# Performance work log

Hardware: AMD Instinct MI355X
Metric: run time of the kernel (lower is better)

Reference implementation:

```python
import jax, jax.numpy as jnp
import numpy as np

GROUPS = 32
EPS = 1e-6

def groupnorm(x, gamma, beta):
    b, c, h, w = x.shape
    xg = x.reshape(b, GROUPS, c // GROUPS, h, w)
    mu = xg.mean(axis=(2, 3, 4), keepdims=True)
    var = xg.var(axis=(2, 3, 4), keepdims=True)
    xn = ((xg - mu) / jnp.sqrt(var + EPS)).reshape(b, c, h, w)
    return xn * gamma[None, :, None, None] + beta[None, :, None, None]

def conv1x1(x, w, b):
    return jnp.einsum('oc,bchw->bohw', w, x) + b[None, :, None, None]

def attn_branch(xn, wq, bq, wk, bk, v_flat, scale):
    q = conv1x1(xn, wq, bq)
    k = conv1x1(xn, wk, bk)
    b_, c, h, w = q.shape
    qf = q.reshape(b_, c, h * w)   # b c n
    kf = k.reshape(b_, c, h * w)   # b c n
    scores = jnp.einsum('bci,bcj->bij', qf, kf) * scale  # b n n
    attn = jax.nn.softmax(scores, axis=2)
    out = jnp.einsum('bcj,bij->bci', v_flat, attn)       # b c n
    return out.reshape(b_, c, h, w)

def setup_inputs() -> dict:
    key = jax.random.key(0)
    ks = jax.random.split(key, 14)
    B, C, H, W = 4, 64, 64, 64
    R = C // 16  # SE reduction
    s = 0.05
    return {
        'x1': jax.random.normal(ks[0], (B, C, H, W), jnp.float32),
        'x2': jax.random.normal(ks[1], (B, C, H, W), jnp.float32),
        'se_w1': jax.random.normal(ks[2], (R, C), jnp.float32) * s,
        'se_w2': jax.random.normal(ks[3], (C, R), jnp.float32) * s,
        'gn_gamma': jnp.ones((C,), jnp.float32),
        'gn_beta': jnp.zeros((C,), jnp.float32),
        'wq': jax.random.normal(ks[4], (C, C), jnp.float32) * s,
        'bq': jnp.zeros((C,), jnp.float32),
        'wk': jax.random.normal(ks[5], (C, C), jnp.float32) * s,
        'bk': jnp.zeros((C,), jnp.float32),
        'wv': jax.random.normal(ks[6], (C, C), jnp.float32) * s,
        'bv': jnp.zeros((C,), jnp.float32),
    }

def reference(x1, x2, se_w1, se_w2, gn_gamma, gn_beta, wq, bq, wk, bk, wv, bv):
    x = x1 + x2
    # SE channel attention (ends in sigmoid), then an EXTRA sigmoid as in source
    y = x.mean(axis=(2, 3))                         # b c
    y = jax.nn.relu(y @ se_w1.T)                    # b r
    y = jax.nn.sigmoid(y @ se_w2.T)                 # b c
    se = x * y[:, :, None, None]
    ch_w = jax.nn.sigmoid(se)
    xn = groupnorm(x, gn_gamma, gn_beta)
    v = conv1x1(xn, wv, bv)
    b_, c, h, w = v.shape
    v_flat = v.reshape(b_, c, h * w)
    scale = 1.0 / jnp.sqrt(jnp.float32(c))
    # source reuses q1/k1 convs for BOTH branches
    h1 = attn_branch(groupnorm(x1, gn_gamma, gn_beta), wq, bq, wk, bk, v_flat, scale)
    h2 = attn_branch(groupnorm(x2, gn_gamma, gn_beta), wq, bq, wk, bk, v_flat, scale)
    return 2.0 * h1 * ch_w + 2.0 * h2 * (1.0 - ch_w)
```

## Files before the change

kernel.cpp:

```cpp
#include <hip/hip_runtime.h>

#define STATS_OFF 0
#define AD_OFF    20480
#define SEY_OFF   26624
#define BIAS_OFF  27648
#define WQB_OFF   32768
#define WKB_OFF   40960
#define WVB_OFF   49152
#define Q_OFF     57344
#define K_OFF     (Q_OFF + 4194304)
#define V_OFF     (K_OFF + 4194304)
#define PO_OFF    (V_OFF + 2097152)

#define QSCALE 0.18033688f

typedef __attribute__((ext_vector_type(8))) short  short8;
typedef __attribute__((ext_vector_type(4))) short  s16x4;
typedef __attribute__((ext_vector_type(2))) unsigned int u32x2;
typedef __attribute__((ext_vector_type(4))) float  f32x4;

#if __has_builtin(__builtin_amdgcn_mfma_f32_16x16x16bf16_1k)
#define HAS_1K 1
#else
#define HAS_1K 0
#endif

#if __has_builtin(__builtin_amdgcn_exp2f)
__device__ inline float fexp2(float x) { return __builtin_amdgcn_exp2f(x); }
#else
__device__ inline float fexp2(float x) { return exp2f(x); }
#endif

__device__ inline ushort f2b(float f) {
  return (ushort)((__float_as_uint(f) + 0x8000u) >> 16);
}
__device__ inline unsigned pack2(float x, float y) {
  unsigned ux = __float_as_uint(x) + 0x8000u;
  unsigned uy = __float_as_uint(y) + 0x8000u;
  return __builtin_amdgcn_perm(uy, ux, 0x07060302);
}
__device__ inline float b2f(ushort u) { return __uint_as_float(((unsigned)u) << 16); }

__device__ inline f32x4 mfma16(short8 a, short8 b, f32x4 c) {
  return __builtin_amdgcn_mfma_f32_16x16x32_bf16(a, b, c, 0, 0, 0);
}

__device__ inline float wsum64(float v) {
  #pragma unroll
  for (int o = 32; o > 0; o >>= 1) v += __shfl_down(v, o, 64);
  return v;
}

__global__ __launch_bounds__(256) void sc_stats(const float* __restrict__ x1,
                                                const float* __restrict__ x2,
                                                float* __restrict__ stats) {
  int blk = blockIdx.x;
  int bc = blk >> 2, chunk = blk & 3;
  const float4* p1 = (const float4*)(x1 + (size_t)bc * 4096 + chunk * 1024);
  const float4* p2 = (const float4*)(x2 + (size_t)bc * 4096 + chunk * 1024);
  float4 a = p1[threadIdx.x], b = p2[threadIdx.x];
  float s1 = a.x + a.y + a.z + a.w;
  float q1 = a.x*a.x + a.y*a.y + a.z*a.z + a.w*a.w;
  float s2 = b.x + b.y + b.z + b.w;
  float q2 = b.x*b.x + b.y*b.y + b.z*b.z + b.w*b.w;
  float p12 = a.x*b.x + a.y*b.y + a.z*b.z + a.w*b.w;
  s1 = wsum64(s1); q1 = wsum64(q1); s2 = wsum64(s2); q2 = wsum64(q2); p12 = wsum64(p12);
  __shared__ float red[4][5];
  int w = threadIdx.x >> 6, ln = threadIdx.x & 63;
  if (ln == 0) { red[w][0] = s1; red[w][1] = q1; red[w][2] = s2; red[w][3] = q2; red[w][4] = p12; }
  __syncthreads();
  if (threadIdx.x < 5) {
    float acc = 0;
    #pragma unroll
    for (int ww = 0; ww < 4; ww++) acc += red[ww][threadIdx.x];
    stats[(size_t)blk * 5 + threadIdx.x] = acc;
  }
}

__global__ __launch_bounds__(256) void sc_prep(const float* __restrict__ stats,
                                               const float* __restrict__ w1,
                                               const float* __restrict__ w2,
                                               const float* __restrict__ gamma,
                                               const float* __restrict__ beta,
                                               const float* __restrict__ wq, const float* __restrict__ bq,
                                               const float* __restrict__ wk, const float* __restrict__ bk,
                                               const float* __restrict__ wv, const float* __restrict__ bv,
                                               float* __restrict__ ad, float* __restrict__ sey,
                                               float* __restrict__ biasbuf,
                                               ushort* __restrict__ wqb, ushort* __restrict__ wkb,
                                               ushort* __restrict__ wvb) {
  int t = threadIdx.x; int b = t >> 6, c = t & 63;
  float s1 = 0, q1 = 0, s2 = 0, q2 = 0, p12 = 0;
  #pragma unroll
  for (int ch = 0; ch < 4; ch++) {
    const float* sp = stats + (size_t)(t * 4 + ch) * 5;
    s1 += sp[0]; q1 += sp[1]; s2 += sp[2]; q2 += sp[3]; p12 += sp[4];
  }
  float sx = s1 + s2, qx = q1 + q2 + 2.f * p12;
  __shared__ float smu[256], sS[3][256], sQ[3][256], sy[16], sdd[3][256];
  smu[t] = sx * (1.f / 4096.f);
  sS[0][t] = sx; sQ[0][t] = qx; sS[1][t] = s1; sQ[1][t] = q1; sS[2][t] = s2; sQ[2][t] = q2;
  __syncthreads();
  if (t < 16) {
    int bb = t >> 2, r = t & 3; float acc = 0.f;
    for (int cc = 0; cc < 64; cc++) acc += w1[r*64+cc] * smu[bb*64+cc];
    sy[t] = fmaxf(acc, 0.f);
  }
  __syncthreads();
  float acc = 0.f;
  #pragma unroll
  for (int r = 0; r < 4; r++) acc += w2[c*4+r] * sy[b*4+r];
  sey[t] = 1.f / (1.f + fexp2(-acc * 1.44269504f));
  int prt = t ^ 1;
  float g = gamma[c], bt = beta[c];
  #pragma unroll
  for (int s = 0; s < 3; s++) {
    float S = sS[s][t] + sS[s][prt], Q = sQ[s][t] + sQ[s][prt];
    float mean = S * (1.f / 8192.f);
    float var  = Q * (1.f / 8192.f) - mean * mean;
    float rstd = rsqrtf(var + 1e-6f);
    float a = g * rstd;
    float d = bt - mean * a;
    ad[((s*256) + t)*2 + 0] = a;
    ad[((s*256) + t)*2 + 1] = d;
    sdd[s][t] = d;
  }
  __syncthreads();
  #pragma unroll
  for (int k = 0; k < 5; k++) {
    int idx = k * 256 + t;
    const float* W; const float* bs; const float* dd; int o; float scale = 1.f;
    if (idx < 256)      { int bb = idx >> 6; o = idx & 63; W = wv; bs = bv; dd = &sdd[0][bb*64]; }
    else if (idx < 768) { int r = idx - 256; int bh = r >> 6; o = r & 63; W = wq; bs = bq;
                          dd = &sdd[1 + (bh & 1)][(bh >> 1)*64]; scale = QSCALE; }
    else                { int r = idx - 768; int bh = r >> 6; o = r & 63; W = wk; bs = bk;
                          dd = &sdd[1 + (bh & 1)][(bh >> 1)*64]; }
    float a2 = bs[o];
    for (int cc = 0; cc < 64; cc++) a2 += W[o*64+cc] * dd[cc];
    biasbuf[idx] = a2 * scale;
  }
  for (int i = t; i < 4096; i += 256) {
    wqb[i] = f2b(wq[i] * QSCALE);
    wkb[i] = f2b(wk[i]);
    wvb[i] = f2b(wv[i]);
  }
}

__global__ __launch_bounds__(256) void sc_proj(const float* __restrict__ x1, const float* __restrict__ x2,
    const float* __restrict__ ad, const float* __restrict__ biasbuf,
    const ushort* __restrict__ wqb, const ushort* __restrict__ wkb, const ushort* __restrict__ wvb,
    ushort* __restrict__ qout, ushort* __restrict__ kout, ushort* __restrict__ vout) {
  int pt = blockIdx.x, src = blockIdx.y, b = blockIdx.z, t = threadIdx.x;
  __shared__ ushort xlds[64 * 66];
  __shared__ ushort olds[64 * 66];
  __shared__ float sbias[2][64];
  if (t < 128) {
    int proj = t >> 6, o = t & 63;
    float bb;
    if (src == 0) bb = (proj == 0) ? biasbuf[b*64 + o] : 0.f;
    else          bb = biasbuf[256 + (proj ? 512 : 0) + (b*2 + src - 1)*64 + o];
    sbias[proj][o] = bb;
  }
  {
    int c = t >> 2, pq = (t & 3) * 16;
    const float* px1 = x1 + ((size_t)(b*64 + c))*4096 + pt*64 + pq;
    const float* px2 = x2 + ((size_t)(b*64 + c))*4096 + pt*64 + pq;
    float av = ad[((src*256) + b*64 + c)*2 + 0];
    #pragma unroll
    for (int k4 = 0; k4 < 4; k4++) {
      float4 v1 = *(const float4*)(px1 + 4*k4);
      float xv[4];
      if (src == 1) { xv[0]=v1.x; xv[1]=v1.y; xv[2]=v1.z; xv[3]=v1.w; }
      else {
        float4 v2 = *(const float4*)(px2 + 4*k4);
        if (src == 2) { xv[0]=v2.x; xv[1]=v2.y; xv[2]=v2.z; xv[3]=v2.w; }
        else { xv[0]=v1.x+v2.x; xv[1]=v1.y+v2.y; xv[2]=v1.z+v2.z; xv[3]=v1.w+v2.w; }
      }
      #pragma unroll
      for (int k = 0; k < 4; k++)
        xlds[(pq + 4*k4 + k)*66 + c] = f2b(av * xv[k]);
    }
  }
  __syncthreads();
  int wave = t >> 6, lane = t & 63, quad = lane >> 4, l15 = lane & 15;
  int orow = t >> 2, ocol = (t & 3) * 16;
  if (src == 0) {
    const ushort* ap = wvb + (wave*16 + l15)*64 + quad*8;
    short8 a0 = *(const short8*)ap;
    short8 a1 = *(const short8*)(ap + 32);
    f32x4 cinit;
    #pragma unroll
    for (int r = 0; r < 4; r++) cinit[r] = sbias[0][wave*16 + quad*4 + r];
    #pragma unroll
    for (int s = 0; s < 4; s++) {
      const ushort* bp = xlds + (s*16 + l15)*66 + quad*8;
      short8 b0 = *(const short8*)bp;
      short8 b1 = *(const short8*)(bp + 32);
      f32x4 acc = mfma16(a0, b0, cinit);
      acc = mfma16(a1, b1, acc);
      #pragma unroll
      for (int r = 0; r < 4; r++)
        olds[(wave*16 + quad*4 + r)*66 + s*16 + l15] = f2b(acc[r]);
    }
    __syncthreads();
    uint4 w0 = *(const uint4*)&olds[orow*66 + ocol];
    uint4 w1 = *(const uint4*)&olds[orow*66 + ocol + 8];
    ushort* dst = vout + ((size_t)(b*64 + orow))*4096 + pt*64 + ocol;
    *(uint4*)dst = w0; *(uint4*)(dst + 8) = w1;
  } else {
    int bh = b*2 + (src - 1);
    const ushort* ap = xlds + (wave*16 + l15)*66 + quad*8;
    short8 a0 = *(const short8*)ap;
    short8 a1 = *(const short8*)(ap + 32);
    #pragma unroll
    for (int proj = 0; proj < 2; proj++) {
      const ushort* Wb = proj == 0 ? wqb : wkb;
      ushort* dst = proj == 0 ? qout : kout;
      #pragma unroll
      for (int s = 0; s < 4; s++) {
        const ushort* bp = Wb + (s*16 + l15)*64 + quad*8;
        short8 b0 = *(const short8*)bp;
        short8 b1 = *(const short8*)(bp + 32);
        float bb = sbias[proj][s*16 + l15];
        f32x4 acc = {bb, bb, bb, bb};
        acc = mfma16(a0, b0, acc);
        acc = mfma16(a1, b1, acc);
        #pragma unroll
        for (int r = 0; r < 4; r++)
          olds[(wave*16 + quad*4 + r)*66 + s*16 + l15] = f2b(acc[r]);
      }
      __syncthreads();
      uint4 w0 = *(const uint4*)&olds[orow*66 + ocol];
      uint4 w1 = *(const uint4*)&olds[orow*66 + ocol + 8];
      ushort* dp = dst + ((size_t)bh*4096 + pt*64 + orow)*64 + ocol;
      *(uint4*)dp = w0; *(uint4*)(dp + 8) = w1;
      if (proj == 0) __syncthreads();
    }
  }
}

__global__ __launch_bounds__(256, 4) void sc_flash(const ushort* __restrict__ qg,
                                                   const ushort* __restrict__ kg,
                                                   const ushort* __restrict__ vg,
                                                   ushort* __restrict__ po,
                                                   float* __restrict__ pl,
                                                   int jsbits) {
  int blk = blockIdx.x;
  int bh = blk & 7, rest = blk >> 3;
  int njs = 1 << jsbits, njt = 64 >> jsbits;
  int js = rest & (njs - 1), itile = rest >> jsbits;
  int jbase = js * (njt << 6);
  int b = bh >> 1;
  int t = threadIdx.x, wave = t >> 6, lane = t & 63, quad = lane >> 4, l15 = lane & 15;
  int i0 = itile * 128 + wave * 32;

  __shared__ ushort Klds[64 * 72];
  __shared__ ushort Vlds[64 * 72];
#if !HAS_1K
  __shared__ ushort Plds[4][32 * 72];
#endif

  const ushort* qbase = qg + ((size_t)bh * 4096 + i0 + l15) * 64 + quad * 8;
  short8 Qb[2][2];
  Qb[0][0] = *(const short8*)qbase;
  Qb[0][1] = *(const short8*)(qbase + 32);
  Qb[1][0] = *(const short8*)(qbase + 16 * 64);
  Qb[1][1] = *(const short8*)(qbase + 16 * 64 + 32);

  f32x4 O[2][4]; const f32x4 zero4 = {0.f, 0.f, 0.f, 0.f};
  #pragma unroll
  for (int ib = 0; ib < 2; ib++)
    #pragma unroll
    for (int cb = 0; cb < 4; cb++) O[ib][cb] = zero4;
  float lsum[2] = {0.f, 0.f};

  int sr = t >> 2, sc = (t & 3) * 16;
  const ushort* ksrc = kg + ((size_t)bh * 4096 + jbase + sr) * 64 + sc;
  const ushort* vsrc = vg + ((size_t)(b * 64 + sr)) * 4096 + jbase + sc;
  ushort* kdst = Klds + sr * 72 + sc;
  ushort* vdst = Vlds + sr * 72 + sc;

  uint4 kr0 = *(const uint4*)ksrc, kr1 = *(const uint4*)(ksrc + 8);
  uint4 vr0 = *(const uint4*)vsrc, vr1 = *(const uint4*)(vsrc + 8);
  ksrc += 4096; vsrc += 64;

  #pragma unroll 1
  for (int jt = 0; jt < njt; jt++) {
    __syncthreads();
    *(uint4*)kdst = kr0; *(uint4*)(kdst + 8) = kr1;
    *(uint4*)vdst = vr0; *(uint4*)(vdst + 8) = vr1;
    __syncthreads();
    if (jt + 1 < njt) {
      kr0 = *(const uint4*)ksrc; kr1 = *(const uint4*)(ksrc + 8);
      vr0 = *(const uint4*)vsrc; vr1 = *(const uint4*)(vsrc + 8);
      ksrc += 4096; vsrc += 64;
    }

    f32x4 S[2][4];
    #pragma unroll
    for (int s = 0; s < 4; s++) {
      const ushort* kp = Klds + (s * 16 + l15) * 72 + quad * 8;
      short8 ka0 = *(const short8*)kp;
      short8 ka1 = *(const short8*)(kp + 32);
      #pragma unroll
      for (int ib = 0; ib < 2; ib++) {
        f32x4 acc = mfma16(ka0, Qb[ib][0], zero4);
        S[ib][s] = mfma16(ka1, Qb[ib][1], acc);
      }
    }

#if HAS_1K
    s16x4 Pb[2][4];
#endif
    #pragma unroll
    for (int ib = 0; ib < 2; ib++) {
      #pragma unroll
      for (int s = 0; s < 4; s++) {
        float p0 = fexp2(S[ib][s][0]);
        float p1 = fexp2(S[ib][s][1]);
        float p2 = fexp2(S[ib][s][2]);
        float p3 = fexp2(S[ib][s][3]);
        lsum[ib] += (p0 + p1) + (p2 + p3);
#if HAS_1K
        u32x2 wpk = {pack2(p0, p1), pack2(p2, p3)};
        Pb[ib][s] = __builtin_bit_cast(s16x4, wpk);
#else
        ushort* pw = &Plds[wave][(ib * 16 + l15) * 72 + s * 16 + quad * 4];
        pw[0] = f2b(p0); pw[1] = f2b(p1); pw[2] = f2b(p2); pw[3] = f2b(p3);
#endif
      }
    }

#if HAS_1K
    #pragma unroll
    for (int s = 0; s < 4; s++) {
      #pragma unroll
      for (int cb = 0; cb < 4; cb++) {
        s16x4 vb = *(const s16x4*)(Vlds + (cb * 16 + l15) * 72 + s * 16 + quad * 4);
        O[0][cb] = __builtin_amdgcn_mfma_f32_16x16x16bf16_1k(Pb[0][s], vb, O[0][cb], 0, 0, 0);
        O[1][cb] = __builtin_amdgcn_mfma_f32_16x16x16bf16_1k(Pb[1][s], vb, O[1][cb], 0, 0, 0);
      }
    }
#else
    __threadfence_block();
    #pragma unroll
    for (int ib = 0; ib < 2; ib++) {
      short8 pa0 = *(const short8*)&Plds[wave][(ib * 16 + l15) * 72 + quad * 8];
      short8 pa1 = *(const short8*)&Plds[wave][(ib * 16 + l15) * 72 + quad * 8 + 32];
      #pragma unroll
      for (int cb = 0; cb < 4; cb++) {
        const ushort* vbp = Vlds + (cb * 16 + l15) * 72 + quad * 8;
        short8 v0 = *(const short8*)vbp;
        short8 v1 = *(const short8*)(vbp + 32);
        O[ib][cb] = mfma16(pa0, v0, O[ib][cb]);
        O[ib][cb] = mfma16(pa1, v1, O[ib][cb]);
      }
    }
#endif
  }

  size_t slice = (size_t)(bh * njs + js) * 4096;
  #pragma unroll
  for (int ib = 0; ib < 2; ib++) {
    float lv = lsum[ib];
    lv += __shfl_xor(lv, 16, 64);
    lv += __shfl_xor(lv, 32, 64);
    if (quad == 0) pl[slice + i0 + ib * 16 + l15] = lv;
    #pragma unroll
    for (int cb = 0; cb < 4; cb++)
      #pragma unroll
      for (int r = 0; r < 4; r++)
        po[(slice + i0 + ib * 16 + quad * 4 + r) * 64 + cb * 16 + l15] = f2b(O[ib][cb][r]);
  }
}

__global__ __launch_bounds__(256) void sc_combine(const float* __restrict__ x1, const float* __restrict__ x2,
                                                  const ushort* __restrict__ po, const float* __restrict__ pl,
                                                  const float* __restrict__ sey,
                                                  float* __restrict__ out, int jsbits) {
  int njs = 1 << jsbits;
  int itile = blockIdx.x, b = blockIdx.y, ch = blockIdx.z, t = threadIdx.x;
  __shared__ float hl[2][32 * 65];
  #pragma unroll
  for (int head = 0; head < 2; head++) {
    int bh = b * 2 + head;
    int i = t >> 2, c8 = (t & 3) * 8;
    float sum[8];
    #pragma unroll
    for (int k = 0; k < 8; k++) sum[k] = 0.f;
    float lacc = 0.f;
    for (int js = 0; js < njs; js++) {
      size_t base = ((size_t)(bh * njs + js)) * 4096;
      uint4 u = *(const uint4*)(po + base * 64 + (size_t)(itile * 64 + i) * 64 + ch * 32 + c8);
      const ushort* us = (const ushort*)&u;
      #pragma unroll
      for (int k = 0; k < 8; k++) sum[k] += b2f(us[k]);
      lacc += pl[base + itile * 64 + i];
    }
    float inv = 1.f / lacc;
    #pragma unroll
    for (int k = 0; k < 8; k++) hl[head][(c8 + k) * 65 + i] = sum[k] * inv;
  }
  __syncthreads();
  #pragma unroll
  for (int it = 0; it < 8; it++) {
    int idx = it * 256 + t;
    int cl = idx >> 6, p = idx & 63;
    int c = ch * 32 + cl;
    size_t gi = ((size_t)(b * 64 + c)) * 4096 + itile * 64 + p;
    float xv = x1[gi] + x2[gi];
    float sig = 1.f / (1.f + fexp2(-xv * sey[b * 64 + c] * 1.44269504f));
    float h1 = hl[0][cl * 65 + p], h2 = hl[1][cl * 65 + p];
    out[gi] = 2.f * (h1 * sig + h2 * (1.f - sig));
  }
}

extern "C" void kernel_launch(void* const* d_in, const int* in_sizes, int n_in,
                              void* d_out, int out_size, void* d_ws, size_t ws_size,
                              hipStream_t stream) {
  (void)in_sizes; (void)n_in; (void)out_size;
  const float* x1    = (const float*)d_in[0];
  const float* x2    = (const float*)d_in[1];
  const float* se_w1 = (const float*)d_in[2];
  const float* se_w2 = (const float*)d_in[3];
  const float* gamma = (const float*)d_in[4];
  const float* beta  = (const float*)d_in[5];
  const float* wq    = (const float*)d_in[6];
  const float* bq    = (const float*)d_in[7];
  const float* wk    = (const float*)d_in[8];
  const float* bk    = (const float*)d_in[9];
  const float* wv    = (const float*)d_in[10];
  const float* bv    = (const float*)d_in[11];
  float* out = (float*)d_out;
  char* ws = (char*)d_ws;
  float*  stats = (float*)(ws + STATS_OFF);
  float*  ad    = (float*)(ws + AD_OFF);
  float*  sey   = (float*)(ws + SEY_OFF);
  float*  biasb = (float*)(ws + BIAS_OFF);
  ushort* wqb   = (ushort*)(ws + WQB_OFF);
  ushort* wkb   = (ushort*)(ws + WKB_OFF);
  ushort* wvb   = (ushort*)(ws + WVB_OFF);
  ushort* qb    = (ushort*)(ws + Q_OFF);
  ushort* kb    = (ushort*)(ws + K_OFF);
  ushort* vb    = (ushort*)(ws + V_OFF);

  int jsbits = 1;
  for (int jb = 3; jb >= 2; jb--) {
    size_t need = (size_t)PO_OFF + ((size_t)8 * 4096 * 64 * 2 + (size_t)8 * 4096 * 4) * (1u << jb);
    if (ws_size >= need) { jsbits = jb; break; }
  }
  int njs = 1 << jsbits;
  ushort* pob = (ushort*)(ws + PO_OFF);
  float*  plb = (float*)(ws + PO_OFF + (size_t)8 * njs * 4096 * 64 * 2);

  sc_stats  <<<1024, 256, 0, stream>>>(x1, x2, stats);
  sc_prep   <<<1, 256, 0, stream>>>(stats, se_w1, se_w2, gamma, beta,
                                    wq, bq, wk, bk, wv, bv,
                                    ad, sey, biasb, wqb, wkb, wvb);
  sc_proj   <<<dim3(64, 3, 4), 256, 0, stream>>>(x1, x2, ad, biasb,
                                                 wqb, wkb, wvb, qb, kb, vb);
  sc_flash  <<<8 * 32 * njs, 256, 0, stream>>>(qb, kb, vb, pob, plb, jsbits);
  sc_combine<<<dim3(64, 4, 2), 256, 0, stream>>>(x1, x2, pob, plb, sey, out, jsbits);
}
```

Baseline: 178.8 us.

## Enlarge flash query tile, swizzle LDS, and redistribute weight prep across kernels

```diff
diff --git a/kernel.cpp b/kernel.cpp
--- a/kernel.cpp
+++ b/kernel.cpp
@@ -3,7 +3,6 @@
 #define STATS_OFF 0
 #define AD_OFF    20480
 #define SEY_OFF   26624
-#define BIAS_OFF  27648
 #define WQB_OFF   32768
 #define WKB_OFF   40960
 #define WVB_OFF   49152
@@ -13,17 +12,12 @@
 #define PO_OFF    (V_OFF + 2097152)
 
 #define QSCALE 0.18033688f
+#define SWZ(r) ((((r) & 7) << 3) ^ (((r) & 8) << 1))
 
 typedef __attribute__((ext_vector_type(8))) short  short8;
 typedef __attribute__((ext_vector_type(4))) short  s16x4;
 typedef __attribute__((ext_vector_type(2))) unsigned int u32x2;
 typedef __attribute__((ext_vector_type(4))) float  f32x4;
-
-#if __has_builtin(__builtin_amdgcn_mfma_f32_16x16x16bf16_1k)
-#define HAS_1K 1
-#else
-#define HAS_1K 0
-#endif
 
 #if __has_builtin(__builtin_amdgcn_exp2f)
 __device__ inline float fexp2(float x) { return __builtin_amdgcn_exp2f(x); }
@@ -53,7 +47,13 @@
 
 __global__ __launch_bounds__(256) void sc_stats(const float* __restrict__ x1,
                                                 const float* __restrict__ x2,
-                                                float* __restrict__ stats) {
+                                                float* __restrict__ stats,
+                                                const float* __restrict__ wq,
+                                                const float* __restrict__ wk,
+                                                const float* __restrict__ wv,
+                                                ushort* __restrict__ wqb,
+                                                ushort* __restrict__ wkb,
+                                                ushort* __restrict__ wvb) {
   int blk = blockIdx.x;
   int bc = blk >> 2, chunk = blk & 3;
   const float4* p1 = (const float4*)(x1 + (size_t)bc * 4096 + chunk * 1024);
@@ -75,6 +75,13 @@
     for (int ww = 0; ww < 4; ww++) acc += red[ww][threadIdx.x];
     stats[(size_t)blk * 5 + threadIdx.x] = acc;
   }
+  if (blk >= 976) {
+    int idx = (blk - 976) * 256 + threadIdx.x;
+    int arr = idx >> 12, e = idx & 4095;
+    if (arr == 0)      wqb[e] = f2b(wq[e] * QSCALE);
+    else if (arr == 1) wkb[e] = f2b(wk[e]);
+    else               wvb[e] = f2b(wv[e]);
+  }
 }
 
 __global__ __launch_bounds__(256) void sc_prep(const float* __restrict__ stats,
@@ -82,13 +89,7 @@
                                                const float* __restrict__ w2,
                                                const float* __restrict__ gamma,
                                                const float* __restrict__ beta,
-                                               const float* __restrict__ wq, const float* __restrict__ bq,
-                                               const float* __restrict__ wk, const float* __restrict__ bk,
-                                               const float* __restrict__ wv, const float* __restrict__ bv,
-                                               float* __restrict__ ad, float* __restrict__ sey,
-                                               float* __restrict__ biasbuf,
-                                               ushort* __restrict__ wqb, ushort* __restrict__ wkb,
-                                               ushort* __restrict__ wvb) {
+                                               float* __restrict__ ad, float* __restrict__ sey) {
   int t = threadIdx.x; int b = t >> 6, c = t & 63;
   float s1 = 0, q1 = 0, s2 = 0, q2 = 0, p12 = 0;
   #pragma unroll
@@ -97,7 +98,7 @@
     s1 += sp[0]; q1 += sp[1]; s2 += sp[2]; q2 += sp[3]; p12 += sp[4];
   }
   float sx = s1 + s2, qx = q1 + q2 + 2.f * p12;
-  __shared__ float smu[256], sS[3][256], sQ[3][256], sy[16], sdd[3][256];
+  __shared__ float smu[256], sS[3][256], sQ[3][256], sy[16];
   smu[t] = sx * (1.f / 4096.f);
   sS[0][t] = sx; sQ[0][t] = qx; sS[1][t] = s1; sQ[1][t] = q1; sS[2][t] = s2; sQ[2][t] = q2;
   __syncthreads();
@@ -120,47 +121,24 @@
     float var  = Q * (1.f / 8192.f) - mean * mean;
     float rstd = rsqrtf(var + 1e-6f);
     float a = g * rstd;
-    float d = bt - mean * a;
     ad[((s*256) + t)*2 + 0] = a;
-    ad[((s*256) + t)*2 + 1] = d;
-    sdd[s][t] = d;
-  }
-  __syncthreads();
-  #pragma unroll
-  for (int k = 0; k < 5; k++) {
-    int idx = k * 256 + t;
-    const float* W; const float* bs; const float* dd; int o; float scale = 1.f;
-    if (idx < 256)      { int bb = idx >> 6; o = idx & 63; W = wv; bs = bv; dd = &sdd[0][bb*64]; }
-    else if (idx < 768) { int r = idx - 256; int bh = r >> 6; o = r & 63; W = wq; bs = bq;
-                          dd = &sdd[1 + (bh & 1)][(bh >> 1)*64]; scale = QSCALE; }
-    else                { int r = idx - 768; int bh = r >> 6; o = r & 63; W = wk; bs = bk;
-                          dd = &sdd[1 + (bh & 1)][(bh >> 1)*64]; }
-    float a2 = bs[o];
-    for (int cc = 0; cc < 64; cc++) a2 += W[o*64+cc] * dd[cc];
-    biasbuf[idx] = a2 * scale;
-  }
-  for (int i = t; i < 4096; i += 256) {
-    wqb[i] = f2b(wq[i] * QSCALE);
-    wkb[i] = f2b(wk[i]);
-    wvb[i] = f2b(wv[i]);
+    ad[((s*256) + t)*2 + 1] = bt - mean * a;
   }
 }
 
 __global__ __launch_bounds__(256) void sc_proj(const float* __restrict__ x1, const float* __restrict__ x2,
-    const float* __restrict__ ad, const float* __restrict__ biasbuf,
+    const float* __restrict__ ad,
+    const float* __restrict__ wq, const float* __restrict__ bq,
+    const float* __restrict__ wk, const float* __restrict__ bk,
+    const float* __restrict__ wv, const float* __restrict__ bv,
     const ushort* __restrict__ wqb, const ushort* __restrict__ wkb, const ushort* __restrict__ wvb,
     ushort* __restrict__ qout, ushort* __restrict__ kout, ushort* __restrict__ vout) {
   int pt = blockIdx.x, src = blockIdx.y, b = blockIdx.z, t = threadIdx.x;
   __shared__ ushort xlds[64 * 66];
   __shared__ ushort olds[64 * 66];
-  __shared__ float sbias[2][64];
-  if (t < 128) {
-    int proj = t >> 6, o = t & 63;
-    float bb;
-    if (src == 0) bb = (proj == 0) ? biasbuf[b*64 + o] : 0.f;
-    else          bb = biasbuf[256 + (proj ? 512 : 0) + (b*2 + src - 1)*64 + o];
-    sbias[proj][o] = bb;
-  }
+  __shared__ float sd[64], sbias[2][64];
+  if (t < 64) sd[t] = ad[((src*256) + b*64 + t)*2 + 1];
+  __syncthreads();
   {
     int c = t >> 2, pq = (t & 3) * 16;
     const float* px1 = x1 + ((size_t)(b*64 + c))*4096 + pt*64 + pq;
@@ -180,6 +158,16 @@
       for (int k = 0; k < 4; k++)
         xlds[(pq + 4*k4 + k)*66 + c] = f2b(av * xv[k]);
     }
+  }
+  int nbias = (src == 0) ? 64 : 128;
+  if (t < nbias) {
+    int proj = t >> 6, o = t & 63;
+    const float* W  = (src == 0) ? wv : (proj == 0 ? wq : wk);
+    const float* bs = (src == 0) ? bv : (proj == 0 ? bq : bk);
+    float acc = bs[o];
+    for (int cc = 0; cc < 64; cc++) acc += W[o*64+cc] * sd[cc];
+    if (src != 0 && proj == 0) acc *= QSCALE;
+    sbias[proj][o] = acc;
   }
   __syncthreads();
   int wave = t >> 6, lane = t & 63, quad = lane >> 4, l15 = lane & 15;
@@ -239,7 +227,7 @@
   }
 }
 
-__global__ __launch_bounds__(256, 4) void sc_flash(const ushort* __restrict__ qg,
+__global__ __launch_bounds__(256, 2) void sc_flash(const ushort* __restrict__ qg,
                                                    const ushort* __restrict__ kg,
                                                    const ushort* __restrict__ vg,
                                                    ushort* __restrict__ po,
@@ -252,33 +240,35 @@
   int jbase = js * (njt << 6);
   int b = bh >> 1;
   int t = threadIdx.x, wave = t >> 6, lane = t & 63, quad = lane >> 4, l15 = lane & 15;
-  int i0 = itile * 128 + wave * 32;
-
-  __shared__ ushort Klds[64 * 72];
-  __shared__ ushort Vlds[64 * 72];
-#if !HAS_1K
-  __shared__ ushort Plds[4][32 * 72];
-#endif
-
-  const ushort* qbase = qg + ((size_t)bh * 4096 + i0 + l15) * 64 + quad * 8;
-  short8 Qb[2][2];
-  Qb[0][0] = *(const short8*)qbase;
-  Qb[0][1] = *(const short8*)(qbase + 32);
-  Qb[1][0] = *(const short8*)(qbase + 16 * 64);
-  Qb[1][1] = *(const short8*)(qbase + 16 * 64 + 32);
-
-  f32x4 O[2][4]; const f32x4 zero4 = {0.f, 0.f, 0.f, 0.f};
-  #pragma unroll
-  for (int ib = 0; ib < 2; ib++)
+  int i0 = itile * 256 + wave * 64;
+
+  __shared__ ushort Klds[64 * 64];
+  __shared__ ushort Vlds[64 * 64];
+
+  short8 Qb[4][2];
+  #pragma unroll
+  for (int ib = 0; ib < 4; ib++) {
+    const ushort* qp = qg + ((size_t)bh * 4096 + i0 + ib * 16 + l15) * 64 + quad * 8;
+    Qb[ib][0] = *(const short8*)qp;
+    Qb[ib][1] = *(const short8*)(qp + 32);
+  }
+
+  f32x4 O[4][4]; const f32x4 zero4 = {0.f, 0.f, 0.f, 0.f};
+  #pragma unroll
+  for (int ib = 0; ib < 4; ib++)
     #pragma unroll
     for (int cb = 0; cb < 4; cb++) O[ib][cb] = zero4;
-  float lsum[2] = {0.f, 0.f};
+  float lsum[4] = {0.f, 0.f, 0.f, 0.f};
 
   int sr = t >> 2, sc = (t & 3) * 16;
+  int swzs = SWZ(sr);
+  int swzl = SWZ(l15);
   const ushort* ksrc = kg + ((size_t)bh * 4096 + jbase + sr) * 64 + sc;
   const ushort* vsrc = vg + ((size_t)(b * 64 + sr)) * 4096 + jbase + sc;
-  ushort* kdst = Klds + sr * 72 + sc;
-  ushort* vdst = Vlds + sr * 72 + sc;
+  ushort* kd0 = Klds + sr * 64 + (sc ^ swzs);
+  ushort* kd1 = Klds + sr * 64 + ((sc + 8) ^ swzs);
+  ushort* vd0 = Vlds + sr * 64 + (sc ^ swzs);
+  ushort* vd1 = Vlds + sr * 64 + ((sc + 8) ^ swzs);
 
   uint4 kr0 = *(const uint4*)ksrc, kr1 = *(const uint4*)(ksrc + 8);
   uint4 vr0 = *(const uint4*)vsrc, vr1 = *(const uint4*)(vsrc + 8);
@@ -287,8 +277,8 @@
   #pragma unroll 1
   for (int jt = 0; jt < njt; jt++) {
     __syncthreads();
-    *(uint4*)kdst = kr0; *(uint4*)(kdst + 8) = kr1;
-    *(uint4*)vdst = vr0; *(uint4*)(vdst + 8) = vr1;
+    *(uint4*)kd0 = kr0; *(uint4*)kd1 = kr1;
+    *(uint4*)vd0 = vr0; *(uint4*)vd1 = vr1;
     __syncthreads();
     if (jt + 1 < njt) {
       kr0 = *(const uint4*)ksrc; kr1 = *(const uint4*)(ksrc + 8);
@@ -296,72 +286,40 @@
       ksrc += 4096; vsrc += 64;
     }
 
-    f32x4 S[2][4];
     #pragma unroll
     for (int s = 0; s < 4; s++) {
-      const ushort* kp = Klds + (s * 16 + l15) * 72 + quad * 8;
-      short8 ka0 = *(const short8*)kp;
-      short8 ka1 = *(const short8*)(kp + 32);
-      #pragma unroll
-      for (int ib = 0; ib < 2; ib++) {
+      int rowK = (s * 16 + l15) * 64;
+      short8 ka0 = *(const short8*)&Klds[rowK + ((quad * 8) ^ swzl)];
+      short8 ka1 = *(const short8*)&Klds[rowK + ((quad * 8 + 32) ^ swzl)];
+      f32x4 S[4];
+      #pragma unroll
+      for (int ib = 0; ib < 4; ib++) {
         f32x4 acc = mfma16(ka0, Qb[ib][0], zero4);
-        S[ib][s] = mfma16(ka1, Qb[ib][1], acc);
+        S[ib] = mfma16(ka1, Qb[ib][1], acc);
       }
-    }
-
-#if HAS_1K
-    s16x4 Pb[2][4];
-#endif
-    #pragma unroll
-    for (int ib = 0; ib < 2; ib++) {
-      #pragma unroll
-      for (int s = 0; s < 4; s++) {
-        float p0 = fexp2(S[ib][s][0]);
-        float p1 = fexp2(S[ib][s][1]);
-        float p2 = fexp2(S[ib][s][2]);
-        float p3 = fexp2(S[ib][s][3]);
+      s16x4 vbf[4];
+      #pragma unroll
+      for (int cb = 0; cb < 4; cb++)
+        vbf[cb] = *(const s16x4*)&Vlds[(cb * 16 + l15) * 64 + ((s * 16 + quad * 4) ^ swzl)];
+      #pragma unroll
+      for (int ib = 0; ib < 4; ib++) {
+        float p0 = fexp2(S[ib][0]);
+        float p1 = fexp2(S[ib][1]);
+        float p2 = fexp2(S[ib][2]);
+        float p3 = fexp2(S[ib][3]);
         lsum[ib] += (p0 + p1) + (p2 + p3);
-#if HAS_1K
         u32x2 wpk = {pack2(p0, p1), pack2(p2, p3)};
-        Pb[ib][s] = __builtin_bit_cast(s16x4, wpk);
-#else
-        ushort* pw = &Plds[wave][(ib * 16 + l15) * 72 + s * 16 + quad * 4];
-        pw[0] = f2b(p0); pw[1] = f2b(p1); pw[2] = f2b(p2); pw[3] = f2b(p3);
-#endif
+        s16x4 Pb = __builtin_bit_cast(s16x4, wpk);
+        #pragma unroll
+        for (int cb = 0; cb < 4; cb++)
+          O[ib][cb] = __builtin_amdgcn_mfma_f32_16x16x16bf16_1k(Pb, vbf[cb], O[ib][cb], 0, 0, 0);
       }
     }
-
-#if HAS_1K
-    #pragma unroll
-    for (int s = 0; s < 4; s++) {
-      #pragma unroll
-      for (int cb = 0; cb < 4; cb++) {
-        s16x4 vb = *(const s16x4*)(Vlds + (cb * 16 + l15) * 72 + s * 16 + quad * 4);
-        O[0][cb] = __builtin_amdgcn_mfma_f32_16x16x16bf16_1k(Pb[0][s], vb, O[0][cb], 0, 0, 0);
-        O[1][cb] = __builtin_amdgcn_mfma_f32_16x16x16bf16_1k(Pb[1][s], vb, O[1][cb], 0, 0, 0);
-      }
-    }
-#else
-    __threadfence_block();
-    #pragma unroll
-    for (int ib = 0; ib < 2; ib++) {
-      short8 pa0 = *(const short8*)&Plds[wave][(ib * 16 + l15) * 72 + quad * 8];
-      short8 pa1 = *(const short8*)&Plds[wave][(ib * 16 + l15) * 72 + quad * 8 + 32];
-      #pragma unroll
-      for (int cb = 0; cb < 4; cb++) {
-        const ushort* vbp = Vlds + (cb * 16 + l15) * 72 + quad * 8;
-        short8 v0 = *(const short8*)vbp;
-        short8 v1 = *(const short8*)(vbp + 32);
-        O[ib][cb] = mfma16(pa0, v0, O[ib][cb]);
-        O[ib][cb] = mfma16(pa1, v1, O[ib][cb]);
-      }
-    }
-#endif
   }
 
   size_t slice = (size_t)(bh * njs + js) * 4096;
   #pragma unroll
-  for (int ib = 0; ib < 2; ib++) {
+  for (int ib = 0; ib < 4; ib++) {
     float lv = lsum[ib];
     lv += __shfl_xor(lv, 16, 64);
     lv += __shfl_xor(lv, 32, 64);
@@ -436,7 +394,6 @@
   float*  stats = (float*)(ws + STATS_OFF);
   float*  ad    = (float*)(ws + AD_OFF);
   float*  sey   = (float*)(ws + SEY_OFF);
-  float*  biasb = (float*)(ws + BIAS_OFF);
   ushort* wqb   = (ushort*)(ws + WQB_OFF);
   ushort* wkb   = (ushort*)(ws + WKB_OFF);
   ushort* wvb   = (ushort*)(ws + WVB_OFF);
@@ -453,12 +410,11 @@
   ushort* pob = (ushort*)(ws + PO_OFF);
   float*  plb = (float*)(ws + PO_OFF + (size_t)8 * njs * 4096 * 64 * 2);
 
-  sc_stats  <<<1024, 256, 0, stream>>>(x1, x2, stats);
-  sc_prep   <<<1, 256, 0, stream>>>(stats, se_w1, se_w2, gamma, beta,
-                                    wq, bq, wk, bk, wv, bv,
-                                    ad, sey, biasb, wqb, wkb, wvb);
-  sc_proj   <<<dim3(64, 3, 4), 256, 0, stream>>>(x1, x2, ad, biasb,
+  sc_stats  <<<1024, 256, 0, stream>>>(x1, x2, stats, wq, wk, wv, wqb, wkb, wvb);
+  sc_prep   <<<1, 256, 0, stream>>>(stats, se_w1, se_w2, gamma, beta, ad, sey);
+  sc_proj   <<<dim3(64, 3, 4), 256, 0, stream>>>(x1, x2, ad,
+                                                 wq, bq, wk, bk, wv, bv,
                                                  wqb, wkb, wvb, qb, kb, vb);
-  sc_flash  <<<8 * 32 * njs, 256, 0, stream>>>(qb, kb, vb, pob, plb, jsbits);
+  sc_flash  <<<8 * 16 * njs, 256, 0, stream>>>(qb, kb, vb, pob, plb, jsbits);
   sc_combine<<<dim3(64, 4, 2), 256, 0, stream>>>(x1, x2, pob, plb, sey, out, jsbits);
 }
```

After: 151.7 us. -15.2%, faster.
